# Optimization experiments

Measured on AMD Instinct MI355X. Metric: run time of the kernel, lower is better.

Reference implementation:

```python
import jax, jax.numpy as jnp
import numpy as np

N_AA, N_CG = 262144, 65536
F_AA, F_CG = 16, 32
H = 128
E_CC, E_CA, E_AC = 262144, 524288, 524288
B = 64  # number of graphs in the batch
LN_EPS = 1e-5


def setup_inputs() -> dict:
    key = jax.random.key(0)
    ks = jax.random.split(key, 32)
    inp = {}
    inp['h_aa0'] = jax.random.normal(ks[0], (N_AA, F_AA), jnp.float32)
    inp['h_cg0'] = jax.random.normal(ks[1], (N_CG, F_CG), jnp.float32)
    inp['src_cc'] = jax.random.randint(ks[2], (E_CC,), 0, N_CG, jnp.int32)
    inp['dst_cc'] = jax.random.randint(ks[3], (E_CC,), 0, N_CG, jnp.int32)
    inp['src_ca'] = jax.random.randint(ks[4], (E_CA,), 0, N_CG, jnp.int32)
    inp['dst_ca'] = jax.random.randint(ks[5], (E_CA,), 0, N_AA, jnp.int32)
    inp['src_ac'] = jax.random.randint(ks[6], (E_AC,), 0, N_AA, jnp.int32)
    inp['dst_ac'] = jax.random.randint(ks[7], (E_AC,), 0, N_CG, jnp.int32)
    inp['graph_id'] = jnp.sort(jax.random.randint(ks[8], (N_AA,), 0, B, jnp.int32))
    def W(k, fi, fo):
        return jax.random.normal(k, (fi, fo), jnp.float32) * 0.05
    z = lambda n: jnp.zeros((n,), jnp.float32)
    o = lambda n: jnp.ones((n,), jnp.float32)
    # input MLPs (no skip)
    inp['W_cg0'], inp['b_cg0'], inp['g_cg0'], inp['be_cg0'] = W(ks[9], F_CG, H), z(H), o(H), z(H)
    inp['W_aa0'], inp['b_aa0'], inp['g_aa0'], inp['be_aa0'] = W(ks[10], F_AA, H), z(H), o(H), z(H)
    # GraphConv cg_to_cg
    inp['W_cc'], inp['b_cc'] = W(ks[11], H, H), z(H)
    # nodewise MLP (applied to aa due to source bug), skip connection
    inp['W_m1'], inp['b_m1'], inp['g_m1'], inp['be_m1'] = W(ks[12], H, H), z(H), o(H), z(H)
    # GraphConv cg_to_aa
    inp['W_ca'], inp['b_ca'] = W(ks[13], H, H), z(H)
    # nodewise MLP on aa, skip
    inp['W_m2'], inp['b_m2'], inp['g_m2'], inp['be_m2'] = W(ks[14], H, H), z(H), o(H), z(H)
    # GraphConv aa_to_cg
    inp['W_ac'], inp['b_ac'] = W(ks[15], H, H), z(H)
    # final nodewise MLP on aa (activation None, LN)
    inp['W_f'], inp['b_f'], inp['g_f'], inp['be_f'] = W(ks[16], H, H), z(H), o(H), z(H)
    return inp


def _layer_norm(h, g, be):
    mu = h.mean(-1, keepdims=True)
    var = ((h - mu) ** 2).mean(-1, keepdims=True)
    return (h - mu) * jax.lax.rsqrt(var + LN_EPS) * g + be


def _mlp(x, Wt, b, g, be, act=True, skip=False):
    h = x @ Wt + b
    if act:
        h = jax.nn.elu(h)
    if skip:
        h = h + x
    return _layer_norm(h, g, be)


def _gconv(h_src, src, dst, n_src, n_dst, Wt, b):
    # DGL GraphConv, norm='both': D_dst^{-1/2} A D_src^{-1/2} X W + b, ELU
    ones = jnp.ones(src.shape[0], h_src.dtype)
    d_out = jnp.clip(jax.ops.segment_sum(ones, src, num_segments=n_src), 1.0) ** -0.5
    d_in = jnp.clip(jax.ops.segment_sum(ones, dst, num_segments=n_dst), 1.0) ** -0.5
    msg = (h_src * d_out[:, None])[src]          # [E, H] gather
    agg = jax.ops.segment_sum(msg, dst, num_segments=n_dst)  # [n_dst, H] scatter-add
    return jax.nn.elu((agg * d_in[:, None]) @ Wt + b)


def reference(h_aa0, h_cg0, src_cc, dst_cc, src_ca, dst_ca, src_ac, dst_ac, graph_id,
              W_cg0, b_cg0, g_cg0, be_cg0, W_aa0, b_aa0, g_aa0, be_aa0,
              W_cc, b_cc, W_m1, b_m1, g_m1, be_m1, W_ca, b_ca,
              W_m2, b_m2, g_m2, be_m2, W_ac, b_ac, W_f, b_f, g_f, be_f):
    n_aa, n_cg = h_aa0.shape[0], h_cg0.shape[0]
    # input embedding MLPs
    h_cg = _mlp(h_cg0, W_cg0, b_cg0, g_cg0, be_cg0)
    h_aa = _mlp(h_aa0, W_aa0, b_aa0, g_aa0, be_aa0)
    # cg_to_cg conv (+ identity skip from HeteroGraphConv sum aggregate)
    h_cg = _gconv(h_cg, src_cc, dst_cc, n_cg, n_cg, W_cc, b_cc) + h_cg
    # 'cg' nodewise MLP — applied to aa nodes (source bug reproduced)
    h_aa = _mlp(h_aa, W_m1, b_m1, g_m1, be_m1, skip=True)
    # cg_to_aa conv
    h_aa = _gconv(h_cg, src_ca, dst_ca, n_cg, n_aa, W_ca, b_ca) + h_aa
    # 'aa' nodewise MLP
    h_aa = _mlp(h_aa, W_m2, b_m2, g_m2, be_m2, skip=True)
    # aa_to_cg conv
    h_cg = _gconv(h_aa, src_ac, dst_ac, n_aa, n_cg, W_ac, b_ac) + h_cg
    # final nodewise layer on pooling level 'aa' (no activation, LN)
    h_aa = _mlp(h_aa, W_f, b_f, g_f, be_f, act=False)
    # mean pooling per graph
    sums = jax.ops.segment_sum(h_aa, graph_id, num_segments=B)      # [B, H]
    counts = jax.ops.segment_sum(jnp.ones((n_aa, 1), h_aa.dtype), graph_id, num_segments=B)
    out = sums / jnp.clip(counts, 1.0)
    return out, counts
```

## Files before the change

kernel.cpp:

```cpp
#include <hip/hip_runtime.h>

using ushort = unsigned short;

#define DEVFN static __device__ __forceinline__

constexpr int H = 128;
constexpr int N_AA = 262144, N_CG = 65536;
constexpr int E_CC = 262144, E_CA = 524288;
constexpr int B_GR = 64;

typedef __attribute__((ext_vector_type(8))) short bf16x8;
typedef __attribute__((ext_vector_type(4))) float f32x4;

DEVFN float elu(float x) { return x > 0.f ? x : __expf(x) - 1.f; }

DEVFN float bf2f(ushort s) { return __uint_as_float(((unsigned)s) << 16); }
DEVFN ushort f2bf(float f) {
  unsigned u = __float_as_uint(f);
  return (ushort)((u + 0x7FFFu + ((u >> 16) & 1u)) >> 16);
}
DEVFN ushort4 pack4(const f32x4& a) {
  return make_ushort4(f2bf(a[0]), f2bf(a[1]), f2bf(a[2]), f2bf(a[3]));
}

DEVFN void fma4(float4& c, float a, float4 w) {
  c.x += a * w.x; c.y += a * w.y; c.z += a * w.z; c.w += a * w.w;
}

__global__ void hist4_kernel(const int* __restrict__ src_cc, const int* __restrict__ dst_cc,
                             const int* __restrict__ src_ca, const int* __restrict__ dst_ca,
                             int* __restrict__ c_scc, int* __restrict__ c_dcc,
                             int* __restrict__ c_sca, int* __restrict__ c_dca) {
  int i = blockIdx.x * blockDim.x + threadIdx.x;
  int stride = gridDim.x * blockDim.x;
  const int T = 2 * E_CC + 2 * E_CA;
  for (; i < T; i += stride) {
    const int* a; int* c; int j = i;
    if (j < E_CC) { a = src_cc; c = c_scc; }
    else if (j < 2 * E_CC) { a = dst_cc; c = c_dcc; j -= E_CC; }
    else if (j < 2 * E_CC + E_CA) { a = src_ca; c = c_sca; j -= 2 * E_CC; }
    else { a = dst_ca; c = c_dca; j -= 2 * E_CC + E_CA; }
    atomicAdd(&c[a[j]], 1);
  }
}

__global__ void graph_count_kernel(const int* __restrict__ gid, int n, int* __restrict__ counts) {
  int b = threadIdx.x;
  auto lb = [&](int v) {
    int lo = 0, hi = n;
    while (lo < hi) { int m = (lo + hi) >> 1; if (gid[m] < v) lo = m + 1; else hi = m; }
    return lo;
  };
  int s = lb(b), e = lb(b + 1);
  counts[b] = e - s;
}

__global__ void deg_all_kernel(const int* __restrict__ cnt, float* __restrict__ d) {
  int i = blockIdx.x * blockDim.x + threadIdx.x;
  int c = cnt[i]; if (c < 1) c = 1;
  d[i] = rsqrtf((float)c);
}

__global__ void wprep_kernel(const float* __restrict__ w0, const float* __restrict__ w1,
                             const float* __restrict__ w2, const float* __restrict__ w3,
                             const float* __restrict__ w4,
                             ushort* __restrict__ o0, ushort* __restrict__ o1,
                             ushort* __restrict__ o2, ushort* __restrict__ o3,
                             ushort* __restrict__ o4,
                             const float* __restrict__ wa, ushort* __restrict__ oa) {
  int idx = blockIdx.x * 256 + threadIdx.x;
  if (idx < 81920) {
    int which = idx >> 14, id = idx & 16383;
    const float* W = which == 0 ? w0 : which == 1 ? w1 : which == 2 ? w2 : which == 3 ? w3 : w4;
    ushort* O = which == 0 ? o0 : which == 1 ? o1 : which == 2 ? o2 : which == 3 ? o3 : o4;
    int r = id >> 7, j = id & 127;
    int k = (j - ((r & 15) << 3)) & 127;
    O[id] = f2bf(W[k * 128 + r]);
  } else if (idx < 86016) {
    int id = idx - 81920;
    int n = id >> 5, k = id & 31;
    oa[id] = (k < 16) ? f2bf(wa[k * 128 + n]) : (ushort)0;
  }
}

__global__ void scan1_kernel(const int* __restrict__ in_cc, int* __restrict__ out_cc,
                             const int* __restrict__ in_ca, int* __restrict__ out_ca,
                             int* __restrict__ bsum) {
  __shared__ int l[256];
  int b = blockIdx.x, tid = threadIdx.x;
  const int* in; int* out; int bi;
  if (b < 64) { in = in_cc; out = out_cc; bi = b; } else { in = in_ca; out = out_ca; bi = b - 64; }
  int base = bi * 1024 + tid * 4;
  int4 v = *(const int4*)&in[base];
  int s = v.x + v.y + v.z + v.w;
  l[tid] = s; __syncthreads();
  for (int off = 1; off < 256; off <<= 1) {
    int t = (tid >= off) ? l[tid - off] : 0;
    __syncthreads();
    if (tid >= off) l[tid] += t;
    __syncthreads();
  }
  int excl = l[tid] - s;
  if (tid == 255) bsum[b] = l[255];
  int4 o; o.x = excl; o.y = o.x + v.x; o.z = o.y + v.y; o.w = o.z + v.z;
  *(int4*)&out[base] = o;
}

__global__ void scan2_kernel(int* __restrict__ bsum) {
  __shared__ int l[256];
  int b = blockIdx.x, tid = threadIdx.x;
  int* bs = bsum + (b ? 64 : 0);
  int nb = b ? 256 : 64;
  int v = (tid < nb) ? bs[tid] : 0;
  l[tid] = v; __syncthreads();
  for (int off = 1; off < 256; off <<= 1) {
    int t = (tid >= off) ? l[tid - off] : 0;
    __syncthreads();
    if (tid >= off) l[tid] += t;
    __syncthreads();
  }
  if (tid < nb) bs[tid] = l[tid] - v;
}

__global__ void scan3_kernel(int* __restrict__ offs_cc, int* __restrict__ cur_cc,
                             int* __restrict__ offs_ca, int* __restrict__ cur_ca,
                             const int* __restrict__ bsum) {
  int i = blockIdx.x * blockDim.x + threadIdx.x;
  if (i < N_CG) {
    int o = offs_cc[i] + bsum[i >> 10];
    offs_cc[i] = o; cur_cc[i] = o;
  } else if (i < N_CG + N_AA) {
    int j = i - N_CG;
    int o = offs_ca[j] + bsum[64 + (j >> 10)];
    offs_ca[j] = o; cur_ca[j] = o;
  }
}

__global__ void place2_kernel(const int* __restrict__ src_cc, const int* __restrict__ dst_cc,
                              const int* __restrict__ src_ca, const int* __restrict__ dst_ca,
                              int* __restrict__ cur_cc, int* __restrict__ sorted_cc,
                              int* __restrict__ cur_ca, int* __restrict__ sorted_ca) {
  int i = blockIdx.x * blockDim.x + threadIdx.x;
  int stride = gridDim.x * blockDim.x;
  for (; i < E_CC + E_CA; i += stride) {
    if (i < E_CC) {
      int d = dst_cc[i];
      int slot = atomicAdd(&cur_cc[d], 1);
      sorted_cc[slot] = src_cc[i];
    } else {
      int j = i - E_CC;
      int d = dst_ca[j];
      int slot = atomicAdd(&cur_ca[d], 1);
      sorted_ca[slot] = src_ca[j];
    }
  }
}

__global__ __launch_bounds__(256) void gather_kernel(
    const ushort* __restrict__ h, const int* __restrict__ sorted_src,
    const int* __restrict__ offs, const int* __restrict__ cnt,
    const float* __restrict__ dout, const float* __restrict__ din,
    ushort* __restrict__ out, int ndst) {
  int lane = threadIdx.x & 31;
  int g0 = (blockIdx.x * blockDim.x + threadIdx.x) >> 5;
  int gstride = (gridDim.x * blockDim.x) >> 5;
  for (int d = g0; d < ndst; d += gstride) {
    int o = offs[d], c = cnt[d];
    float ax = 0.f, ay = 0.f, az = 0.f, aw = 0.f;
    for (int e = o; e < o + c; ++e) {
      int s = sorted_src[e];
      float w = dout[s];
      ushort4 u = *(const ushort4*)&h[(size_t)s * H + lane * 4];
      ax += w * bf2f(u.x); ay += w * bf2f(u.y);
      az += w * bf2f(u.z); aw += w * bf2f(u.w);
    }
    float di = din[d];
    ushort4 r = make_ushort4(f2bf(ax * di), f2bf(ay * di), f2bf(az * di), f2bf(aw * di));
    *(ushort4*)&out[(size_t)d * H + lane * 4] = r;
  }
}


DEVFN void stage_w(const ushort* __restrict__ g, ushort* l, int tid) {
  for (int i = tid; i < 2048; i += 512)
    *((uint4*)l + i) = *((const uint4*)g + i);
}

DEVFN void load_bfrag(const ushort* __restrict__ A, size_t mrow, int q, bf16x8 bfr[4]) {
#pragma unroll
  for (int ks = 0; ks < 4; ks++)
    bfr[ks] = *(const bf16x8*)(A + mrow + ks * 32 + q * 8);
}

DEVFN void load_skip_raw(const ushort* __restrict__ skip, size_t mrow, int q, ushort4 sk[8]) {
#pragma unroll
  for (int nf = 0; nf < 8; nf++)
    sk[nf] = *(const ushort4*)&skip[mrow + nf * 16 + q * 4];
}

DEVFN void gemm128_lds(const ushort* __restrict__ Wlds, const bf16x8 bfr[4], f32x4 acc[8], int t, int q) {
#pragma unroll
  for (int ks = 0; ks < 4; ks++) {
    int coff = (ks * 64 + q * 16 + t * 16) & 255;
#pragma unroll
    for (int nf = 0; nf < 8; nf++) {
      bf16x8 wv = *(const bf16x8*)((const char*)Wlds + (nf * 16 + t) * 256 + coff);
      acc[nf] = __builtin_amdgcn_mfma_f32_16x16x32_bf16(wv, bfr[ks], acc[nf], 0, 0, 0);
    }
  }
}

DEVFN void chained_gemm(const ushort* __restrict__ Wlds, char* cbb, int t, int q,
                        const f32x4 ain[8], f32x4 acc[8]) {
  const int tb = t * 8;
  char* row = cbb + t * 128;
#pragma unroll
  for (int half = 0; half < 2; half++) {
    asm volatile("s_waitcnt lgkmcnt(0)" ::: "memory");
#pragma unroll
    for (int nfl = 0; nfl < 4; nfl++) {
      int off = (nfl * 32 + q * 8 + tb) & 127;
      *(ushort4*)(row + off) = pack4(ain[half * 4 + nfl]);
    }
    asm volatile("s_waitcnt lgkmcnt(0)" ::: "memory");
#pragma unroll
    for (int ksl = 0; ksl < 2; ksl++) {
      int ks = half * 2 + ksl;
      uint2 lo = *(const uint2*)(row + ((ksl * 64 + q * 16 + tb) & 127));
      uint2 hi = *(const uint2*)(row + ((ksl * 64 + q * 16 + 8 + tb) & 127));
      union { uint4 u; bf16x8 v; } b;
      b.u = make_uint4(lo.x, lo.y, hi.x, hi.y);
      int coff = (ks * 64 + q * 16 + t * 16) & 255;
#pragma unroll
      for (int nf = 0; nf < 8; nf++) {
        bf16x8 wv = *(const bf16x8*)((const char*)Wlds + (nf * 16 + t) * 256 + coff);
        acc[nf] = __builtin_amdgcn_mfma_f32_16x16x32_bf16(wv, b.v, acc[nf], 0, 0, 0);
      }
    }
  }
}

template<bool ACT>
DEVFN void bias_act(f32x4 a[8], const float* __restrict__ bias, int q) {
#pragma unroll
  for (int nf = 0; nf < 8; nf++) {
    float4 bb = *(const float4*)&bias[nf * 16 + q * 4];
    a[nf][0] += bb.x; a[nf][1] += bb.y; a[nf][2] += bb.z; a[nf][3] += bb.w;
    if constexpr (ACT) {
#pragma unroll
      for (int e = 0; e < 4; e++) a[nf][e] = elu(a[nf][e]);
    }
  }
}

DEVFN void add_reg(f32x4 a[8], const f32x4 b[8]) {
#pragma unroll
  for (int nf = 0; nf < 8; nf++)
#pragma unroll
    for (int e = 0; e < 4; e++) a[nf][e] += b[nf][e];
}

DEVFN void add_skip_r(f32x4 a[8], const ushort4 sk[8]) {
#pragma unroll
  for (int nf = 0; nf < 8; nf++) {
    a[nf][0] += bf2f(sk[nf].x); a[nf][1] += bf2f(sk[nf].y);
    a[nf][2] += bf2f(sk[nf].z); a[nf][3] += bf2f(sk[nf].w);
  }
}

DEVFN void layernorm(f32x4 a[8], const float* __restrict__ gamma, const float* __restrict__ beta, int q) {
  float s = 0.f;
#pragma unroll
  for (int nf = 0; nf < 8; nf++) s += a[nf][0] + a[nf][1] + a[nf][2] + a[nf][3];
  s += __shfl_xor(s, 16); s += __shfl_xor(s, 32);
  float mu = s * 0.0078125f;
  float d = 0.f;
#pragma unroll
  for (int nf = 0; nf < 8; nf++)
#pragma unroll
    for (int e = 0; e < 4; e++) { float x = a[nf][e] - mu; d += x * x; }
  d += __shfl_xor(d, 16); d += __shfl_xor(d, 32);
  float rs = rsqrtf(d * 0.0078125f + 1e-5f);
#pragma unroll
  for (int nf = 0; nf < 8; nf++) {
    float4 gg = *(const float4*)&gamma[nf * 16 + q * 4];
    float4 be = *(const float4*)&beta[nf * 16 + q * 4];
    a[nf][0] = (a[nf][0] - mu) * rs * gg.x + be.x;
    a[nf][1] = (a[nf][1] - mu) * rs * gg.y + be.y;
    a[nf][2] = (a[nf][2] - mu) * rs * gg.z + be.z;
    a[nf][3] = (a[nf][3] - mu) * rs * gg.w + be.w;
  }
}

DEVFN void store_row(ushort* __restrict__ out, size_t mrow, const f32x4 a[8], int q) {
#pragma unroll
  for (int nf = 0; nf < 8; nf++)
    *(ushort4*)&out[mrow + nf * 16 + q * 4] = pack4(a[nf]);
}

__global__ __launch_bounds__(512) void fused_aa_kernel(
    const float* __restrict__ h0, int ngrp,
    const ushort* __restrict__ Wp,
    const float* __restrict__ b0, const float* __restrict__ g0, const float* __restrict__ be0,
    const ushort* __restrict__ Wswm1,
    const float* __restrict__ b1, const float* __restrict__ g1, const float* __restrict__ be1,
    ushort* __restrict__ out) {
  __shared__ ushort Wm1[16384];
  __shared__ ushort chain[8 * 1024];
  int tid = threadIdx.x;
  stage_w(Wswm1, Wm1, tid);
  int lane = tid & 63, wave = tid >> 6;
  int t = lane & 15, q = lane >> 4;
  char* cbb = (char*)chain + wave * 2048;
  bf16x8 wfa[8];
#pragma unroll
  for (int nf = 0; nf < 8; nf++)
    wfa[nf] = *(const bf16x8*)(Wp + (nf * 16 + t) * 32 + q * 8);

  int grp = blockIdx.x;
  float4 c0, c1;
  if (grp < ngrp && q < 2) {
    const float* src = h0 + ((size_t)(grp * 128 + wave * 16 + t) << 4) + (q << 3);
    c0 = *(const float4*)src; c1 = *(const float4*)(src + 4);
  }
  __syncthreads();

  for (; grp < ngrp;) {
    int nxt = grp + gridDim.x;
    float4 n0, n1;
    if (nxt < ngrp && q < 2) {
      const float* src = h0 + ((size_t)(nxt * 128 + wave * 16 + t) << 4) + (q << 3);
      n0 = *(const float4*)src; n1 = *(const float4*)(src + 4);
    }
    size_t mrow = (size_t)(grp * 128 + wave * 16 + t) * H;
    bf16x8 bf0;
    if (q < 2) {
      bf0[0] = (short)f2bf(c0.x); bf0[1] = (short)f2bf(c0.y);
      bf0[2] = (short)f2bf(c0.z); bf0[3] = (short)f2bf(c0.w);
      bf0[4] = (short)f2bf(c1.x); bf0[5] = (short)f2bf(c1.y);
      bf0[6] = (short)f2bf(c1.z); bf0[7] = (short)f2bf(c1.w);
    } else {
#pragma unroll
      for (int e = 0; e < 8; e++) bf0[e] = 0;
    }
    f32x4 a0[8];
#pragma unroll
    for (int nf = 0; nf < 8; nf++) a0[nf] = (f32x4){0.f, 0.f, 0.f, 0.f};
#pragma unroll
    for (int nf = 0; nf < 8; nf++)
      a0[nf] = __builtin_amdgcn_mfma_f32_16x16x32_bf16(wfa[nf], bf0, a0[nf], 0, 0, 0);
    bias_act<true>(a0, b0, q);
    layernorm(a0, g0, be0, q);

    f32x4 a1[8];
#pragma unroll
    for (int nf = 0; nf < 8; nf++) a1[nf] = (f32x4){0.f, 0.f, 0.f, 0.f};
    chained_gemm(Wm1, cbb, t, q, a0, a1);
    bias_act<true>(a1, b1, q);
    add_reg(a1, a0);
    layernorm(a1, g1, be1, q);
    store_row(out, mrow, a1, q);

    grp = nxt; c0 = n0; c1 = n1;
  }
}

__global__ __launch_bounds__(512) void cc_gemm_kernel(
    const ushort* __restrict__ A, int ngrp,
    const ushort* __restrict__ Wsw, const float* __restrict__ bias,
    const ushort* __restrict__ skip, ushort* __restrict__ out) {
  __shared__ ushort Wl[16384];
  int tid = threadIdx.x;
  stage_w(Wsw, Wl, tid);
  int lane = tid & 63, wave = tid >> 6;
  int t = lane & 15, q = lane >> 4;
  __syncthreads();
  for (int grp = blockIdx.x; grp < ngrp; grp += gridDim.x) {
    size_t mrow = (size_t)(grp * 128 + wave * 16 + t) * H;
    bf16x8 bfr[4];
    load_bfrag(A, mrow, q, bfr);
    ushort4 sk[8];
    load_skip_raw(skip, mrow, q, sk);
    f32x4 a[8];
#pragma unroll
    for (int nf = 0; nf < 8; nf++) a[nf] = (f32x4){0.f, 0.f, 0.f, 0.f};
    gemm128_lds(Wl, bfr, a, t, q);
    bias_act<true>(a, bias, q);
    add_skip_r(a, sk);
    store_row(out, mrow, a, q);
  }
}

__global__ __launch_bounds__(512) void fused3_kernel(
    const ushort* __restrict__ A, const ushort* __restrict__ Hbskip, int ngrp,
    const ushort* __restrict__ Wswca, const float* __restrict__ bca,
    const ushort* __restrict__ Wswm2, const float* __restrict__ bm2,
    const float* __restrict__ gm2, const float* __restrict__ bem2,
    const ushort* __restrict__ Wswf, const float* __restrict__ bf,
    const float* __restrict__ gf, const float* __restrict__ bef,
    ushort* __restrict__ out) {
  __shared__ ushort Wca[16384], Wm2[16384], Wf[16384];
  __shared__ ushort chain[8 * 1024];
  int tid = threadIdx.x;
  stage_w(Wswca, Wca, tid);
  stage_w(Wswm2, Wm2, tid);
  stage_w(Wswf, Wf, tid);
  int lane = tid & 63, wave = tid >> 6;
  int t = lane & 15, q = lane >> 4;
  char* cbb = (char*)chain + wave * 2048;

  int grp = blockIdx.x;
  bf16x8 bfr[4];
  ushort4 sk[8];
  if (grp < ngrp) {
    size_t mrow = (size_t)(grp * 128 + wave * 16 + t) * H;
    load_bfrag(A, mrow, q, bfr);
    load_skip_raw(Hbskip, mrow, q, sk);
  }
  __syncthreads();

  for (; grp < ngrp;) {
    int nxt = grp + gridDim.x;
    bf16x8 nbfr[4];
    ushort4 nsk[8];
    if (nxt < ngrp) {
      size_t nrow = (size_t)(nxt * 128 + wave * 16 + t) * H;
      load_bfrag(A, nrow, q, nbfr);
      load_skip_raw(Hbskip, nrow, q, nsk);
    }
    size_t mrow = (size_t)(grp * 128 + wave * 16 + t) * H;

    f32x4 a1[8];
#pragma unroll
    for (int nf = 0; nf < 8; nf++) a1[nf] = (f32x4){0.f, 0.f, 0.f, 0.f};
    gemm128_lds(Wca, bfr, a1, t, q);
    bias_act<true>(a1, bca, q);
    add_skip_r(a1, sk);

    f32x4 a2[8];
#pragma unroll
    for (int nf = 0; nf < 8; nf++) a2[nf] = (f32x4){0.f, 0.f, 0.f, 0.f};
    chained_gemm(Wm2, cbb, t, q, a1, a2);
    bias_act<true>(a2, bm2, q);
    add_reg(a2, a1);
    layernorm(a2, gm2, bem2, q);

    f32x4 a3[8];
#pragma unroll
    for (int nf = 0; nf < 8; nf++) a3[nf] = (f32x4){0.f, 0.f, 0.f, 0.f};
    chained_gemm(Wf, cbb, t, q, a2, a3);
    bias_act<false>(a3, bf, q);
    layernorm(a3, gf, bef, q);
    store_row(out, mrow, a3, q);

    grp = nxt;
#pragma unroll
    for (int ks = 0; ks < 4; ks++) bfr[ks] = nbfr[ks];
#pragma unroll
    for (int nf = 0; nf < 8; nf++) sk[nf] = nsk[nf];
  }
}

template<int K, bool ACT, bool LN>
__global__ __launch_bounds__(512) void gemm_fused(
    const float* __restrict__ Av, int ntiles,
    const float* __restrict__ W, const float* __restrict__ bias,
    const float* __restrict__ gamma, const float* __restrict__ beta,
    ushort* __restrict__ out) {
  constexpr int AS = K + 4;
  constexpr int KM = K - 1;
  constexpr int F4R = K / 4;
  __shared__ float Wl[K * H];
  __shared__ float Al[128 * AS];
  int tid = threadIdx.x;

  for (int q = tid; q < K * H / 4; q += 512)
    *(float4*)&Wl[q * 4] = *(const float4*)&W[q * 4];

  int tc = tid & 31, tr = tid >> 5;
  const int rot = (4 * tr) & KM;
  const int c = 4 * tc;
  const float* aBase = Al + (tr * 8) * AS;

  for (int tile = blockIdx.x; tile < ntiles; tile += gridDim.x) {
    int r0 = tile * 128;
    __syncthreads();
    for (int q = tid; q < 128 * F4R; q += 512) {
      int r = q / F4R, cc = (q % F4R) * 4;
      float4 v = *(const float4*)(Av + (size_t)(r0 + r) * K + cc);
      int rr = (4 * (r >> 3)) & KM;
      *(float4*)&Al[r * AS + ((cc + rr) & KM)] = v;
    }
    __syncthreads();

    float4 acc[8];
#pragma unroll
    for (int i = 0; i < 8; i++) acc[i] = make_float4(0.f, 0.f, 0.f, 0.f);

#pragma unroll 2
    for (int k = 0; k < K; k += 4) {
      int kp = (k + rot) & KM;
      float4 av[8];
#pragma unroll
      for (int r8 = 0; r8 < 8; r8++) av[r8] = *(const float4*)(aBase + r8 * AS + kp);
      float4 w0 = *(const float4*)&Wl[(k + 0) * H + c];
      float4 w1 = *(const float4*)&Wl[(k + 1) * H + c];
      float4 w2 = *(const float4*)&Wl[(k + 2) * H + c];
      float4 w3 = *(const float4*)&Wl[(k + 3) * H + c];
#pragma unroll
      for (int r8 = 0; r8 < 8; r8++) {
        float4 a = av[r8];
        fma4(acc[r8], a.x, w0); fma4(acc[r8], a.y, w1);
        fma4(acc[r8], a.z, w2); fma4(acc[r8], a.w, w3);
      }
    }

    float4 bA = *(const float4*)&bias[c];
    float4 gA, beA;
    if constexpr (LN) {
      gA = *(const float4*)&gamma[c];
      beA = *(const float4*)&beta[c];
    }
#pragma unroll
    for (int r8 = 0; r8 < 8; r8++) {
      int r = tr * 8 + r8;
      size_t grow = (size_t)(r0 + r) * H;
      float4 v;
      v.x = acc[r8].x + bA.x; v.y = acc[r8].y + bA.y;
      v.z = acc[r8].z + bA.z; v.w = acc[r8].w + bA.w;
      if constexpr (ACT) {
        v.x = elu(v.x); v.y = elu(v.y); v.z = elu(v.z); v.w = elu(v.w);
      }
      if constexpr (LN) {
        float s = v.x + v.y + v.z + v.w;
        s += __shfl_xor(s, 1); s += __shfl_xor(s, 2);
        s += __shfl_xor(s, 4); s += __shfl_xor(s, 8); s += __shfl_xor(s, 16);
        float mu = s * 0.0078125f;
        float t, d;
        t = v.x - mu; d = t * t;  t = v.y - mu; d += t * t;
        t = v.z - mu; d += t * t; t = v.w - mu; d += t * t;
        d += __shfl_xor(d, 1); d += __shfl_xor(d, 2);
        d += __shfl_xor(d, 4); d += __shfl_xor(d, 8); d += __shfl_xor(d, 16);
        float rs = rsqrtf(d * 0.0078125f + 1e-5f);
        v.x = (v.x - mu) * rs * gA.x + beA.x; v.y = (v.y - mu) * rs * gA.y + beA.y;
        v.z = (v.z - mu) * rs * gA.z + beA.z; v.w = (v.w - mu) * rs * gA.w + beA.w;
      }
      *(ushort4*)&out[grow + c] = make_ushort4(f2bf(v.x), f2bf(v.y), f2bf(v.z), f2bf(v.w));
    }
  }
}

__global__ __launch_bounds__(128) void pool_sum_kernel(const ushort* __restrict__ h,
                                                       const int* __restrict__ gid,
                                                       float* __restrict__ sums) {
  int f = threadIdx.x;
  int chunk = N_AA / gridDim.x;
  int start = blockIdx.x * chunk, end = start + chunk;
  int g = gid[start];
  float acc = 0.f;
  for (int i = start; i < end; ++i) {
    int gi = gid[i];
    if (gi != g) { atomicAdd(&sums[g * H + f], acc); acc = 0.f; g = gi; }
    acc += bf2f(h[(size_t)i * H + f]);
  }
  atomicAdd(&sums[g * H + f], acc);
}

__global__ void pool_final_kernel(const float* __restrict__ sums, const int* __restrict__ counts,
                                  float* __restrict__ out) {
  int b = blockIdx.x, f = threadIdx.x;
  float c = (float)counts[b];
  out[b * H + f] = sums[b * H + f] / fmaxf(c, 1.f);
  if (f == 0) out[B_GR * H + b] = c;
}

extern "C" void kernel_launch(void* const* d_in, const int* in_sizes, int n_in,
                              void* d_out, int out_size, void* d_ws, size_t ws_size,
                              hipStream_t stream) {
  (void)in_sizes; (void)n_in; (void)out_size; (void)ws_size;
  const float* h_aa0 = (const float*)d_in[0];
  const float* h_cg0 = (const float*)d_in[1];
  const int* src_cc = (const int*)d_in[2];
  const int* dst_cc = (const int*)d_in[3];
  const int* src_ca = (const int*)d_in[4];
  const int* dst_ca = (const int*)d_in[5];
  const int* graph_id = (const int*)d_in[8];
  const float* W_cg0 = (const float*)d_in[9];
  const float* b_cg0 = (const float*)d_in[10];
  const float* g_cg0 = (const float*)d_in[11];
  const float* be_cg0 = (const float*)d_in[12];
  const float* W_aa0 = (const float*)d_in[13];
  const float* b_aa0 = (const float*)d_in[14];
  const float* g_aa0 = (const float*)d_in[15];
  const float* be_aa0 = (const float*)d_in[16];
  const float* W_cc = (const float*)d_in[17];
  const float* b_cc = (const float*)d_in[18];
  const float* W_m1 = (const float*)d_in[19];
  const float* b_m1 = (const float*)d_in[20];
  const float* g_m1 = (const float*)d_in[21];
  const float* be_m1 = (const float*)d_in[22];
  const float* W_ca = (const float*)d_in[23];
  const float* b_ca = (const float*)d_in[24];
  const float* W_m2 = (const float*)d_in[25];
  const float* b_m2 = (const float*)d_in[26];
  const float* g_m2 = (const float*)d_in[27];
  const float* be_m2 = (const float*)d_in[28];
  const float* W_f = (const float*)d_in[31];
  const float* b_f = (const float*)d_in[32];
  const float* g_f = (const float*)d_in[33];
  const float* be_f = (const float*)d_in[34];

  char* ws = (char*)d_ws;
  size_t off = 0;
  auto alloc = [&](size_t bytes) -> void* {
    void* p = ws + off;
    off = (off + bytes + 255) & ~(size_t)255;
    return p;
  };
  ushort* cgA = (ushort*)alloc((size_t)N_CG * H * 2);
  ushort* G   = (ushort*)alloc((size_t)N_CG * H * 2);
  ushort* Hb  = (ushort*)alloc((size_t)N_AA * H * 2);
  ushort* AGG = (ushort*)alloc((size_t)N_AA * H * 2);
  int* cnt_s_cc = (int*)alloc((size_t)N_CG * 4);
  int* cnt_d_cc = (int*)alloc((size_t)N_CG * 4);
  int* cnt_s_ca = (int*)alloc((size_t)N_CG * 4);
  int* cnt_d_ca = (int*)alloc((size_t)N_AA * 4);
  float* dout_cc = (float*)alloc((size_t)N_CG * 4);
  float* din_cc  = (float*)alloc((size_t)N_CG * 4);
  float* dout_ca = (float*)alloc((size_t)N_CG * 4);
  float* din_ca  = (float*)alloc((size_t)N_AA * 4);
  int* offs_cc = (int*)alloc((size_t)N_CG * 4);
  int* cur_cc  = (int*)alloc((size_t)N_CG * 4);
  int* offs_ca = (int*)alloc((size_t)N_AA * 4);
  int* cur_ca  = (int*)alloc((size_t)N_AA * 4);
  int* sorted_cc = (int*)alloc((size_t)E_CC * 4);
  int* sorted_ca = (int*)alloc((size_t)E_CA * 4);
  int* bsum = (int*)alloc(320 * 4);
  float* sums = (float*)alloc((size_t)B_GR * H * 4);
  int* counts = (int*)alloc(256);
  ushort* Wsw_cc = (ushort*)alloc(H * H * 2);
  ushort* Wsw_m1 = (ushort*)alloc(H * H * 2);
  ushort* Wsw_ca = (ushort*)alloc(H * H * 2);
  ushort* Wsw_m2 = (ushort*)alloc(H * H * 2);
  ushort* Wsw_f  = (ushort*)alloc(H * H * 2);
  ushort* Wp_aa  = (ushort*)alloc(H * 32 * 2);

  hipMemsetAsync(cnt_s_cc, 0, (size_t)(3 * N_CG + N_AA) * 4, stream);
  hipMemsetAsync(sums, 0, (size_t)B_GR * H * 4, stream);

  wprep_kernel<<<336, 256, 0, stream>>>(W_cc, W_m1, W_ca, W_m2, W_f,
                                        Wsw_cc, Wsw_m1, Wsw_ca, Wsw_m2, Wsw_f,
                                        W_aa0, Wp_aa);
  hist4_kernel<<<2048, 256, 0, stream>>>(src_cc, dst_cc, src_ca, dst_ca,
                                         cnt_s_cc, cnt_d_cc, cnt_s_ca, cnt_d_ca);
  graph_count_kernel<<<1, 64, 0, stream>>>(graph_id, N_AA, counts);
  deg_all_kernel<<<(3 * N_CG + N_AA) / 256, 256, 0, stream>>>(cnt_s_cc, dout_cc);

  scan1_kernel<<<320, 256, 0, stream>>>(cnt_d_cc, offs_cc, cnt_d_ca, offs_ca, bsum);
  scan2_kernel<<<2, 256, 0, stream>>>(bsum);
  scan3_kernel<<<(N_CG + N_AA) / 256, 256, 0, stream>>>(offs_cc, cur_cc, offs_ca, cur_ca, bsum);
  place2_kernel<<<2048, 256, 0, stream>>>(src_cc, dst_cc, src_ca, dst_ca,
                                          cur_cc, sorted_cc, cur_ca, sorted_ca);

  gemm_fused<32, true, true><<<N_CG / 128, 512, 0, stream>>>(
      h_cg0, N_CG / 128, W_cg0, b_cg0, g_cg0, be_cg0, cgA);

  fused_aa_kernel<<<512, 512, 0, stream>>>(
      h_aa0, N_AA / 128, Wp_aa, b_aa0, g_aa0, be_aa0,
      Wsw_m1, b_m1, g_m1, be_m1, Hb);

  gather_kernel<<<N_CG / 8, 256, 0, stream>>>(cgA, sorted_cc, offs_cc, cnt_d_cc, dout_cc, din_cc, G, N_CG);
  cc_gemm_kernel<<<N_CG / 128, 512, 0, stream>>>(G, N_CG / 128, Wsw_cc, b_cc, cgA, G);

  gather_kernel<<<N_AA / 8, 256, 0, stream>>>(G, sorted_ca, offs_ca, cnt_d_ca, dout_ca, din_ca, AGG, N_AA);
  fused3_kernel<<<256, 512, 0, stream>>>(
      AGG, Hb, N_AA / 128,
      Wsw_ca, b_ca, Wsw_m2, b_m2, g_m2, be_m2,
      Wsw_f, b_f, g_f, be_f, AGG);

  pool_sum_kernel<<<1024, 128, 0, stream>>>(AGG, graph_id, sums);
  pool_final_kernel<<<B_GR, 128, 0, stream>>>(sums, counts, (float*)d_out);
}
```

Before: 476.7 us.

## Process two 16-row tiles per wave to reuse LDS weight fragments

Each wave now handles 32 rows instead of 16 in the aa-embedding, cc GEMM and fused3 kernels, so every weight fragment read from LDS feeds two MFMAs, halving LDS weight traffic per row. Chain buffers double to hold both tiles. The fused_aa kernel drops its register prefetch of the next group's input, and fused3 now loads the skip values inside the loop instead of prefetching them. Register pressure roughly doubles for accumulators, which risks lower occupancy or spills. Grid sizes are adjusted accordingly (fused_aa grid raised to 1024 blocks).

```diff
diff --git a/kernel.cpp b/kernel.cpp
--- a/kernel.cpp
+++ b/kernel.cpp
@@ -198,43 +198,56 @@
     sk[nf] = *(const ushort4*)&skip[mrow + nf * 16 + q * 4];
 }
 
-DEVFN void gemm128_lds(const ushort* __restrict__ Wlds, const bf16x8 bfr[4], f32x4 acc[8], int t, int q) {
+DEVFN void gemm128_lds2(const ushort* __restrict__ Wlds,
+                        const bf16x8 b0[4], const bf16x8 b1[4],
+                        f32x4 A0[8], f32x4 A1[8], int t, int q) {
 #pragma unroll
   for (int ks = 0; ks < 4; ks++) {
     int coff = (ks * 64 + q * 16 + t * 16) & 255;
 #pragma unroll
     for (int nf = 0; nf < 8; nf++) {
       bf16x8 wv = *(const bf16x8*)((const char*)Wlds + (nf * 16 + t) * 256 + coff);
-      acc[nf] = __builtin_amdgcn_mfma_f32_16x16x32_bf16(wv, bfr[ks], acc[nf], 0, 0, 0);
-    }
-  }
-}
-
-DEVFN void chained_gemm(const ushort* __restrict__ Wlds, char* cbb, int t, int q,
-                        const f32x4 ain[8], f32x4 acc[8]) {
+      A0[nf] = __builtin_amdgcn_mfma_f32_16x16x32_bf16(wv, b0[ks], A0[nf], 0, 0, 0);
+      A1[nf] = __builtin_amdgcn_mfma_f32_16x16x32_bf16(wv, b1[ks], A1[nf], 0, 0, 0);
+    }
+  }
+}
+
+DEVFN void chained_gemm2(const ushort* __restrict__ Wlds, char* cb0, char* cb1,
+                         int t, int q,
+                         const f32x4 i0[8], const f32x4 i1[8],
+                         f32x4 A0[8], f32x4 A1[8]) {
   const int tb = t * 8;
-  char* row = cbb + t * 128;
+  char* row0 = cb0 + t * 128;
+  char* row1 = cb1 + t * 128;
 #pragma unroll
   for (int half = 0; half < 2; half++) {
     asm volatile("s_waitcnt lgkmcnt(0)" ::: "memory");
 #pragma unroll
     for (int nfl = 0; nfl < 4; nfl++) {
       int off = (nfl * 32 + q * 8 + tb) & 127;
-      *(ushort4*)(row + off) = pack4(ain[half * 4 + nfl]);
+      *(ushort4*)(row0 + off) = pack4(i0[half * 4 + nfl]);
+      *(ushort4*)(row1 + off) = pack4(i1[half * 4 + nfl]);
     }
     asm volatile("s_waitcnt lgkmcnt(0)" ::: "memory");
 #pragma unroll
     for (int ksl = 0; ksl < 2; ksl++) {
       int ks = half * 2 + ksl;
-      uint2 lo = *(const uint2*)(row + ((ksl * 64 + q * 16 + tb) & 127));
-      uint2 hi = *(const uint2*)(row + ((ksl * 64 + q * 16 + 8 + tb) & 127));
-      union { uint4 u; bf16x8 v; } b;
-      b.u = make_uint4(lo.x, lo.y, hi.x, hi.y);
+      int olo = (ksl * 64 + q * 16 + tb) & 127;
+      int ohi = (ksl * 64 + q * 16 + 8 + tb) & 127;
+      uint2 lo0 = *(const uint2*)(row0 + olo);
+      uint2 hi0 = *(const uint2*)(row0 + ohi);
+      uint2 lo1 = *(const uint2*)(row1 + olo);
+      uint2 hi1 = *(const uint2*)(row1 + ohi);
+      union { uint4 u; bf16x8 v; } b0, b1;
+      b0.u = make_uint4(lo0.x, lo0.y, hi0.x, hi0.y);
+      b1.u = make_uint4(lo1.x, lo1.y, hi1.x, hi1.y);
       int coff = (ks * 64 + q * 16 + t * 16) & 255;
 #pragma unroll
       for (int nf = 0; nf < 8; nf++) {
         bf16x8 wv = *(const bf16x8*)((const char*)Wlds + (nf * 16 + t) * 256 + coff);
-        acc[nf] = __builtin_amdgcn_mfma_f32_16x16x32_bf16(wv, b.v, acc[nf], 0, 0, 0);
+        A0[nf] = __builtin_amdgcn_mfma_f32_16x16x32_bf16(wv, b0.v, A0[nf], 0, 0, 0);
+        A1[nf] = __builtin_amdgcn_mfma_f32_16x16x32_bf16(wv, b1.v, A1[nf], 0, 0, 0);
       }
     }
   }
@@ -306,62 +319,70 @@
     const float* __restrict__ b1, const float* __restrict__ g1, const float* __restrict__ be1,
     ushort* __restrict__ out) {
   __shared__ ushort Wm1[16384];
-  __shared__ ushort chain[8 * 1024];
+  __shared__ ushort chain[8 * 2048];
   int tid = threadIdx.x;
   stage_w(Wswm1, Wm1, tid);
   int lane = tid & 63, wave = tid >> 6;
   int t = lane & 15, q = lane >> 4;
-  char* cbb = (char*)chain + wave * 2048;
+  char* cb0 = (char*)chain + wave * 4096;
+  char* cb1 = cb0 + 2048;
   bf16x8 wfa[8];
 #pragma unroll
   for (int nf = 0; nf < 8; nf++)
     wfa[nf] = *(const bf16x8*)(Wp + (nf * 16 + t) * 32 + q * 8);
-
-  int grp = blockIdx.x;
-  float4 c0, c1;
-  if (grp < ngrp && q < 2) {
-    const float* src = h0 + ((size_t)(grp * 128 + wave * 16 + t) << 4) + (q << 3);
-    c0 = *(const float4*)src; c1 = *(const float4*)(src + 4);
-  }
   __syncthreads();
 
-  for (; grp < ngrp;) {
-    int nxt = grp + gridDim.x;
-    float4 n0, n1;
-    if (nxt < ngrp && q < 2) {
-      const float* src = h0 + ((size_t)(nxt * 128 + wave * 16 + t) << 4) + (q << 3);
-      n0 = *(const float4*)src; n1 = *(const float4*)(src + 4);
-    }
-    size_t mrow = (size_t)(grp * 128 + wave * 16 + t) * H;
-    bf16x8 bf0;
-    if (q < 2) {
-      bf0[0] = (short)f2bf(c0.x); bf0[1] = (short)f2bf(c0.y);
-      bf0[2] = (short)f2bf(c0.z); bf0[3] = (short)f2bf(c0.w);
-      bf0[4] = (short)f2bf(c1.x); bf0[5] = (short)f2bf(c1.y);
-      bf0[6] = (short)f2bf(c1.z); bf0[7] = (short)f2bf(c1.w);
-    } else {
-#pragma unroll
-      for (int e = 0; e < 8; e++) bf0[e] = 0;
-    }
-    f32x4 a0[8];
-#pragma unroll
-    for (int nf = 0; nf < 8; nf++) a0[nf] = (f32x4){0.f, 0.f, 0.f, 0.f};
-#pragma unroll
-    for (int nf = 0; nf < 8; nf++)
-      a0[nf] = __builtin_amdgcn_mfma_f32_16x16x32_bf16(wfa[nf], bf0, a0[nf], 0, 0, 0);
-    bias_act<true>(a0, b0, q);
-    layernorm(a0, g0, be0, q);
-
-    f32x4 a1[8];
-#pragma unroll
-    for (int nf = 0; nf < 8; nf++) a1[nf] = (f32x4){0.f, 0.f, 0.f, 0.f};
-    chained_gemm(Wm1, cbb, t, q, a0, a1);
-    bias_act<true>(a1, b1, q);
-    add_reg(a1, a0);
-    layernorm(a1, g1, be1, q);
-    store_row(out, mrow, a1, q);
-
-    grp = nxt; c0 = n0; c1 = n1;
+  for (int grp = blockIdx.x; grp < ngrp; grp += gridDim.x) {
+    int base = grp * 256 + wave * 32;
+    size_t mrow0 = (size_t)(base + t) * H;
+    size_t mrow1 = (size_t)(base + 16 + t) * H;
+
+    bf16x8 bf0[2];
+#pragma unroll
+    for (int g = 0; g < 2; g++) {
+      if (q < 2) {
+        const float* src = h0 + ((size_t)(base + g * 16 + t) << 4) + (q << 3);
+        float4 u0 = *(const float4*)src;
+        float4 u1 = *(const float4*)(src + 4);
+        bf0[g][0] = (short)f2bf(u0.x); bf0[g][1] = (short)f2bf(u0.y);
+        bf0[g][2] = (short)f2bf(u0.z); bf0[g][3] = (short)f2bf(u0.w);
+        bf0[g][4] = (short)f2bf(u1.x); bf0[g][5] = (short)f2bf(u1.y);
+        bf0[g][6] = (short)f2bf(u1.z); bf0[g][7] = (short)f2bf(u1.w);
+      } else {
+#pragma unroll
+        for (int e = 0; e < 8; e++) bf0[g][e] = 0;
+      }
+    }
+    f32x4 a0[2][8];
+#pragma unroll
+    for (int g = 0; g < 2; g++)
+#pragma unroll
+      for (int nf = 0; nf < 8; nf++) a0[g][nf] = (f32x4){0.f, 0.f, 0.f, 0.f};
+#pragma unroll
+    for (int nf = 0; nf < 8; nf++) {
+      a0[0][nf] = __builtin_amdgcn_mfma_f32_16x16x32_bf16(wfa[nf], bf0[0], a0[0][nf], 0, 0, 0);
+      a0[1][nf] = __builtin_amdgcn_mfma_f32_16x16x32_bf16(wfa[nf], bf0[1], a0[1][nf], 0, 0, 0);
+    }
+#pragma unroll
+    for (int g = 0; g < 2; g++) {
+      bias_act<true>(a0[g], b0, q);
+      layernorm(a0[g], g0, be0, q);
+    }
+
+    f32x4 a1[2][8];
+#pragma unroll
+    for (int g = 0; g < 2; g++)
+#pragma unroll
+      for (int nf = 0; nf < 8; nf++) a1[g][nf] = (f32x4){0.f, 0.f, 0.f, 0.f};
+    chained_gemm2(Wm1, cb0, cb1, t, q, a0[0], a0[1], a1[0], a1[1]);
+#pragma unroll
+    for (int g = 0; g < 2; g++) {
+      bias_act<true>(a1[g], b1, q);
+      add_reg(a1[g], a0[g]);
+      layernorm(a1[g], g1, be1, q);
+    }
+    store_row(out, mrow0, a1[0], q);
+    store_row(out, mrow1, a1[1], q);
   }
 }
 
@@ -376,18 +397,28 @@
   int t = lane & 15, q = lane >> 4;
   __syncthreads();
   for (int grp = blockIdx.x; grp < ngrp; grp += gridDim.x) {
-    size_t mrow = (size_t)(grp * 128 + wave * 16 + t) * H;
-    bf16x8 bfr[4];
-    load_bfrag(A, mrow, q, bfr);
-    ushort4 sk[8];
-    load_skip_raw(skip, mrow, q, sk);
-    f32x4 a[8];
-#pragma unroll
-    for (int nf = 0; nf < 8; nf++) a[nf] = (f32x4){0.f, 0.f, 0.f, 0.f};
-    gemm128_lds(Wl, bfr, a, t, q);
-    bias_act<true>(a, bias, q);
-    add_skip_r(a, sk);
-    store_row(out, mrow, a, q);
+    int base = grp * 256 + wave * 32;
+    size_t mrow0 = (size_t)(base + t) * H;
+    size_t mrow1 = (size_t)(base + 16 + t) * H;
+    bf16x8 bfr[2][4];
+    load_bfrag(A, mrow0, q, bfr[0]);
+    load_bfrag(A, mrow1, q, bfr[1]);
+    ushort4 sk[2][8];
+    load_skip_raw(skip, mrow0, q, sk[0]);
+    load_skip_raw(skip, mrow1, q, sk[1]);
+    f32x4 a[2][8];
+#pragma unroll
+    for (int g = 0; g < 2; g++)
+#pragma unroll
+      for (int nf = 0; nf < 8; nf++) a[g][nf] = (f32x4){0.f, 0.f, 0.f, 0.f};
+    gemm128_lds2(Wl, bfr[0], bfr[1], a[0], a[1], t, q);
+#pragma unroll
+    for (int g = 0; g < 2; g++) {
+      bias_act<true>(a[g], bias, q);
+      add_skip_r(a[g], sk[g]);
+    }
+    store_row(out, mrow0, a[0], q);
+    store_row(out, mrow1, a[1], q);
   }
 }
 
@@ -400,64 +431,84 @@
     const float* __restrict__ gf, const float* __restrict__ bef,
     ushort* __restrict__ out) {
   __shared__ ushort Wca[16384], Wm2[16384], Wf[16384];
-  __shared__ ushort chain[8 * 1024];
+  __shared__ ushort chain[8 * 2048];
   int tid = threadIdx.x;
   stage_w(Wswca, Wca, tid);
   stage_w(Wswm2, Wm2, tid);
   stage_w(Wswf, Wf, tid);
   int lane = tid & 63, wave = tid >> 6;
   int t = lane & 15, q = lane >> 4;
-  char* cbb = (char*)chain + wave * 2048;
+  char* cb0 = (char*)chain + wave * 4096;
+  char* cb1 = cb0 + 2048;
 
   int grp = blockIdx.x;
-  bf16x8 bfr[4];
-  ushort4 sk[8];
+  bf16x8 bfr[2][4];
   if (grp < ngrp) {
-    size_t mrow = (size_t)(grp * 128 + wave * 16 + t) * H;
-    load_bfrag(A, mrow, q, bfr);
-    load_skip_raw(Hbskip, mrow, q, sk);
+    int base = grp * 256 + wave * 32;
+    load_bfrag(A, (size_t)(base + t) * H, q, bfr[0]);
+    load_bfrag(A, (size_t)(base + 16 + t) * H, q, bfr[1]);
   }
   __syncthreads();
 
   for (; grp < ngrp;) {
     int nxt = grp + gridDim.x;
-    bf16x8 nbfr[4];
-    ushort4 nsk[8];
+    bf16x8 nbfr[2][4];
     if (nxt < ngrp) {
-      size_t nrow = (size_t)(nxt * 128 + wave * 16 + t) * H;
-      load_bfrag(A, nrow, q, nbfr);
-      load_skip_raw(Hbskip, nrow, q, nsk);
-    }
-    size_t mrow = (size_t)(grp * 128 + wave * 16 + t) * H;
-
-    f32x4 a1[8];
-#pragma unroll
-    for (int nf = 0; nf < 8; nf++) a1[nf] = (f32x4){0.f, 0.f, 0.f, 0.f};
-    gemm128_lds(Wca, bfr, a1, t, q);
-    bias_act<true>(a1, bca, q);
-    add_skip_r(a1, sk);
-
-    f32x4 a2[8];
-#pragma unroll
-    for (int nf = 0; nf < 8; nf++) a2[nf] = (f32x4){0.f, 0.f, 0.f, 0.f};
-    chained_gemm(Wm2, cbb, t, q, a1, a2);
-    bias_act<true>(a2, bm2, q);
-    add_reg(a2, a1);
-    layernorm(a2, gm2, bem2, q);
-
-    f32x4 a3[8];
-#pragma unroll
-    for (int nf = 0; nf < 8; nf++) a3[nf] = (f32x4){0.f, 0.f, 0.f, 0.f};
-    chained_gemm(Wf, cbb, t, q, a2, a3);
-    bias_act<false>(a3, bf, q);
-    layernorm(a3, gf, bef, q);
-    store_row(out, mrow, a3, q);
+      int nb = nxt * 256 + wave * 32;
+      load_bfrag(A, (size_t)(nb + t) * H, q, nbfr[0]);
+      load_bfrag(A, (size_t)(nb + 16 + t) * H, q, nbfr[1]);
+    }
+    int base = grp * 256 + wave * 32;
+    size_t mrow0 = (size_t)(base + t) * H;
+    size_t mrow1 = (size_t)(base + 16 + t) * H;
+    ushort4 sk[2][8];
+    load_skip_raw(Hbskip, mrow0, q, sk[0]);
+    load_skip_raw(Hbskip, mrow1, q, sk[1]);
+
+    f32x4 a1[2][8];
+#pragma unroll
+    for (int g = 0; g < 2; g++)
+#pragma unroll
+      for (int nf = 0; nf < 8; nf++) a1[g][nf] = (f32x4){0.f, 0.f, 0.f, 0.f};
+    gemm128_lds2(Wca, bfr[0], bfr[1], a1[0], a1[1], t, q);
+#pragma unroll
+    for (int g = 0; g < 2; g++) {
+      bias_act<true>(a1[g], bca, q);
+      add_skip_r(a1[g], sk[g]);
+    }
+
+    f32x4 a2[2][8];
+#pragma unroll
+    for (int g = 0; g < 2; g++)
+#pragma unroll
+      for (int nf = 0; nf < 8; nf++) a2[g][nf] = (f32x4){0.f, 0.f, 0.f, 0.f};
+    chained_gemm2(Wm2, cb0, cb1, t, q, a1[0], a1[1], a2[0], a2[1]);
+#pragma unroll
+    for (int g = 0; g < 2; g++) {
+      bias_act<true>(a2[g], bm2, q);
+      add_reg(a2[g], a1[g]);
+      layernorm(a2[g], gm2, bem2, q);
+    }
+
+    f32x4 a3[2][8];
+#pragma unroll
+    for (int g = 0; g < 2; g++)
+#pragma unroll
+      for (int nf = 0; nf < 8; nf++) a3[g][nf] = (f32x4){0.f, 0.f, 0.f, 0.f};
+    chained_gemm2(Wf, cb0, cb1, t, q, a2[0], a2[1], a3[0], a3[1]);
+#pragma unroll
+    for (int g = 0; g < 2; g++) {
+      bias_act<false>(a3[g], bf, q);
+      layernorm(a3[g], gf, bef, q);
+    }
+    store_row(out, mrow0, a3[0], q);
+    store_row(out, mrow1, a3[1], q);
 
     grp = nxt;
 #pragma unroll
-    for (int ks = 0; ks < 4; ks++) bfr[ks] = nbfr[ks];
-#pragma unroll
-    for (int nf = 0; nf < 8; nf++) sk[nf] = nsk[nf];
+    for (int g = 0; g < 2; g++)
+#pragma unroll
+      for (int ks = 0; ks < 4; ks++) bfr[g][ks] = nbfr[g][ks];
   }
 }
 
@@ -665,16 +716,16 @@
   gemm_fused<32, true, true><<<N_CG / 128, 512, 0, stream>>>(
       h_cg0, N_CG / 128, W_cg0, b_cg0, g_cg0, be_cg0, cgA);
 
-  fused_aa_kernel<<<512, 512, 0, stream>>>(
-      h_aa0, N_AA / 128, Wp_aa, b_aa0, g_aa0, be_aa0,
+  fused_aa_kernel<<<1024, 512, 0, stream>>>(
+      h_aa0, N_AA / 256, Wp_aa, b_aa0, g_aa0, be_aa0,
       Wsw_m1, b_m1, g_m1, be_m1, Hb);
 
   gather_kernel<<<N_CG / 8, 256, 0, stream>>>(cgA, sorted_cc, offs_cc, cnt_d_cc, dout_cc, din_cc, G, N_CG);
-  cc_gemm_kernel<<<N_CG / 128, 512, 0, stream>>>(G, N_CG / 128, Wsw_cc, b_cc, cgA, G);
+  cc_gemm_kernel<<<N_CG / 256, 512, 0, stream>>>(G, N_CG / 256, Wsw_cc, b_cc, cgA, G);
 
   gather_kernel<<<N_AA / 8, 256, 0, stream>>>(G, sorted_ca, offs_ca, cnt_d_ca, dout_ca, din_ca, AGG, N_AA);
   fused3_kernel<<<256, 512, 0, stream>>>(
-      AGG, Hb, N_AA / 128,
+      AGG, Hb, N_AA / 256,
       Wsw_ca, b_ca, Wsw_m2, b_m2, g_m2, be_m2,
       Wsw_f, b_f, g_f, be_f, AGG);
 
```

Measured after the change: 559.7 us. 17.4% more time.

## Fuse neighbor gather into conv GEMM kernels and split the aa MLP chain

Applied to the files above, without the earlier changes.

The separate gather kernels are removed. Each destination row's neighbor sum is now built directly in MFMA B-fragment registers inside the cc and ca GEMM kernels, so the aggregated tensor is no longer written to and re-read from memory. The old three-GEMM fused kernel is split into a ca conv kernel and a separate m2+final MLP kernel, which lowers LDS use per block but adds a round trip of the intermediate activations through global memory. It also adds s_setprio around the MFMA loops and raises the grid sizes for the aa MLP and pool kernels. The fused gather has one thread per row doing serial neighbor loops with 32 accumulators, which can cost parallelism, add register pressure and cause load imbalance.

```diff
diff --git a/kernel.cpp b/kernel.cpp
--- a/kernel.cpp
+++ b/kernel.cpp
@@ -156,30 +156,6 @@
   }
 }
 
-__global__ __launch_bounds__(256) void gather_kernel(
-    const ushort* __restrict__ h, const int* __restrict__ sorted_src,
-    const int* __restrict__ offs, const int* __restrict__ cnt,
-    const float* __restrict__ dout, const float* __restrict__ din,
-    ushort* __restrict__ out, int ndst) {
-  int lane = threadIdx.x & 31;
-  int g0 = (blockIdx.x * blockDim.x + threadIdx.x) >> 5;
-  int gstride = (gridDim.x * blockDim.x) >> 5;
-  for (int d = g0; d < ndst; d += gstride) {
-    int o = offs[d], c = cnt[d];
-    float ax = 0.f, ay = 0.f, az = 0.f, aw = 0.f;
-    for (int e = o; e < o + c; ++e) {
-      int s = sorted_src[e];
-      float w = dout[s];
-      ushort4 u = *(const ushort4*)&h[(size_t)s * H + lane * 4];
-      ax += w * bf2f(u.x); ay += w * bf2f(u.y);
-      az += w * bf2f(u.z); aw += w * bf2f(u.w);
-    }
-    float di = din[d];
-    ushort4 r = make_ushort4(f2bf(ax * di), f2bf(ay * di), f2bf(az * di), f2bf(aw * di));
-    *(ushort4*)&out[(size_t)d * H + lane * 4] = r;
-  }
-}
-
 
 DEVFN void stage_w(const ushort* __restrict__ g, ushort* l, int tid) {
   for (int i = tid; i < 2048; i += 512)
@@ -198,7 +174,33 @@
     sk[nf] = *(const ushort4*)&skip[mrow + nf * 16 + q * 4];
 }
 
+DEVFN void gather_bfrag(const ushort* __restrict__ h, const int* __restrict__ sorted,
+                        int o, int c, const float* __restrict__ dout, float di,
+                        int q, bf16x8 bfr[4]) {
+  float acc[4][8];
+#pragma unroll
+  for (int ks = 0; ks < 4; ks++)
+#pragma unroll
+    for (int j = 0; j < 8; j++) acc[ks][j] = 0.f;
+  for (int e = o; e < o + c; ++e) {
+    int s = sorted[e];
+    float w = dout[s];
+    const ushort* row = h + (size_t)s * H + q * 8;
+#pragma unroll
+    for (int ks = 0; ks < 4; ks++) {
+      bf16x8 v = *(const bf16x8*)(row + ks * 32);
+#pragma unroll
+      for (int j = 0; j < 8; j++) acc[ks][j] += w * bf2f((ushort)v[j]);
+    }
+  }
+#pragma unroll
+  for (int ks = 0; ks < 4; ks++)
+#pragma unroll
+    for (int j = 0; j < 8; j++) bfr[ks][j] = (short)f2bf(acc[ks][j] * di);
+}
+
 DEVFN void gemm128_lds(const ushort* __restrict__ Wlds, const bf16x8 bfr[4], f32x4 acc[8], int t, int q) {
+  __builtin_amdgcn_s_setprio(1);
 #pragma unroll
   for (int ks = 0; ks < 4; ks++) {
     int coff = (ks * 64 + q * 16 + t * 16) & 255;
@@ -208,6 +210,7 @@
       acc[nf] = __builtin_amdgcn_mfma_f32_16x16x32_bf16(wv, bfr[ks], acc[nf], 0, 0, 0);
     }
   }
+  __builtin_amdgcn_s_setprio(0);
 }
 
 DEVFN void chained_gemm(const ushort* __restrict__ Wlds, char* cbb, int t, int q,
@@ -231,11 +234,13 @@
       union { uint4 u; bf16x8 v; } b;
       b.u = make_uint4(lo.x, lo.y, hi.x, hi.y);
       int coff = (ks * 64 + q * 16 + t * 16) & 255;
+      __builtin_amdgcn_s_setprio(1);
 #pragma unroll
       for (int nf = 0; nf < 8; nf++) {
         bf16x8 wv = *(const bf16x8*)((const char*)Wlds + (nf * 16 + t) * 256 + coff);
         acc[nf] = __builtin_amdgcn_mfma_f32_16x16x32_bf16(wv, b.v, acc[nf], 0, 0, 0);
       }
+      __builtin_amdgcn_s_setprio(0);
     }
   }
 }
@@ -346,9 +351,11 @@
     f32x4 a0[8];
 #pragma unroll
     for (int nf = 0; nf < 8; nf++) a0[nf] = (f32x4){0.f, 0.f, 0.f, 0.f};
+    __builtin_amdgcn_s_setprio(1);
 #pragma unroll
     for (int nf = 0; nf < 8; nf++)
       a0[nf] = __builtin_amdgcn_mfma_f32_16x16x32_bf16(wfa[nf], bf0, a0[nf], 0, 0, 0);
+    __builtin_amdgcn_s_setprio(0);
     bias_act<true>(a0, b0, q);
     layernorm(a0, g0, be0, q);
 
@@ -365,10 +372,13 @@
   }
 }
 
-__global__ __launch_bounds__(512) void cc_gemm_kernel(
-    const ushort* __restrict__ A, int ngrp,
+__global__ __launch_bounds__(512) void cc_fused_kernel(
+    const ushort* __restrict__ cgA, int ngrp,
+    const int* __restrict__ offs, const int* __restrict__ cnt,
+    const int* __restrict__ sorted, const float* __restrict__ dout,
+    const float* __restrict__ din,
     const ushort* __restrict__ Wsw, const float* __restrict__ bias,
-    const ushort* __restrict__ skip, ushort* __restrict__ out) {
+    ushort* __restrict__ outG) {
   __shared__ ushort Wl[16384];
   int tid = threadIdx.x;
   stage_w(Wsw, Wl, tid);
@@ -376,73 +386,82 @@
   int t = lane & 15, q = lane >> 4;
   __syncthreads();
   for (int grp = blockIdx.x; grp < ngrp; grp += gridDim.x) {
-    size_t mrow = (size_t)(grp * 128 + wave * 16 + t) * H;
+    int nd = grp * 128 + wave * 16 + t;
+    size_t mrow = (size_t)nd * H;
     bf16x8 bfr[4];
-    load_bfrag(A, mrow, q, bfr);
+    gather_bfrag(cgA, sorted, offs[nd], cnt[nd], dout, din[nd], q, bfr);
     ushort4 sk[8];
-    load_skip_raw(skip, mrow, q, sk);
+    load_skip_raw(cgA, mrow, q, sk);
     f32x4 a[8];
 #pragma unroll
     for (int nf = 0; nf < 8; nf++) a[nf] = (f32x4){0.f, 0.f, 0.f, 0.f};
     gemm128_lds(Wl, bfr, a, t, q);
     bias_act<true>(a, bias, q);
     add_skip_r(a, sk);
-    store_row(out, mrow, a, q);
-  }
-}
-
-__global__ __launch_bounds__(512) void fused3_kernel(
-    const ushort* __restrict__ A, const ushort* __restrict__ Hbskip, int ngrp,
-    const ushort* __restrict__ Wswca, const float* __restrict__ bca,
+    store_row(outG, mrow, a, q);
+  }
+}
+
+__global__ __launch_bounds__(512) void ca_fused_kernel(
+    const ushort* __restrict__ G, const ushort* __restrict__ Hbskip, int ngrp,
+    const int* __restrict__ offs, const int* __restrict__ cnt,
+    const int* __restrict__ sorted, const float* __restrict__ dout,
+    const float* __restrict__ din,
+    const ushort* __restrict__ Wsw, const float* __restrict__ bias,
+    ushort* __restrict__ outX) {
+  __shared__ ushort Wl[16384];
+  int tid = threadIdx.x;
+  stage_w(Wsw, Wl, tid);
+  int lane = tid & 63, wave = tid >> 6;
+  int t = lane & 15, q = lane >> 4;
+  __syncthreads();
+  for (int grp = blockIdx.x; grp < ngrp; grp += gridDim.x) {
+    int nd = grp * 128 + wave * 16 + t;
+    size_t mrow = (size_t)nd * H;
+    bf16x8 bfr[4];
+    gather_bfrag(G, sorted, offs[nd], cnt[nd], dout, din[nd], q, bfr);
+    ushort4 sk[8];
+    load_skip_raw(Hbskip, mrow, q, sk);
+    f32x4 a[8];
+#pragma unroll
+    for (int nf = 0; nf < 8; nf++) a[nf] = (f32x4){0.f, 0.f, 0.f, 0.f};
+    gemm128_lds(Wl, bfr, a, t, q);
+    bias_act<true>(a, bias, q);
+    add_skip_r(a, sk);
+    store_row(outX, mrow, a, q);
+  }
+}
+
+__global__ __launch_bounds__(512) void m2f_kernel(
+    const ushort* __restrict__ X, int ngrp,
     const ushort* __restrict__ Wswm2, const float* __restrict__ bm2,
     const float* __restrict__ gm2, const float* __restrict__ bem2,
     const ushort* __restrict__ Wswf, const float* __restrict__ bf,
     const float* __restrict__ gf, const float* __restrict__ bef,
     ushort* __restrict__ out) {
-  __shared__ ushort Wca[16384], Wm2[16384], Wf[16384];
+  __shared__ ushort Wm2[16384], Wf[16384];
   __shared__ ushort chain[8 * 1024];
   int tid = threadIdx.x;
-  stage_w(Wswca, Wca, tid);
   stage_w(Wswm2, Wm2, tid);
   stage_w(Wswf, Wf, tid);
   int lane = tid & 63, wave = tid >> 6;
   int t = lane & 15, q = lane >> 4;
   char* cbb = (char*)chain + wave * 2048;
-
-  int grp = blockIdx.x;
-  bf16x8 bfr[4];
-  ushort4 sk[8];
-  if (grp < ngrp) {
+  __syncthreads();
+
+  for (int grp = blockIdx.x; grp < ngrp; grp += gridDim.x) {
     size_t mrow = (size_t)(grp * 128 + wave * 16 + t) * H;
-    load_bfrag(A, mrow, q, bfr);
-    load_skip_raw(Hbskip, mrow, q, sk);
-  }
-  __syncthreads();
-
-  for (; grp < ngrp;) {
-    int nxt = grp + gridDim.x;
-    bf16x8 nbfr[4];
-    ushort4 nsk[8];
-    if (nxt < ngrp) {
-      size_t nrow = (size_t)(nxt * 128 + wave * 16 + t) * H;
-      load_bfrag(A, nrow, q, nbfr);
-      load_skip_raw(Hbskip, nrow, q, nsk);
-    }
-    size_t mrow = (size_t)(grp * 128 + wave * 16 + t) * H;
-
-    f32x4 a1[8];
-#pragma unroll
-    for (int nf = 0; nf < 8; nf++) a1[nf] = (f32x4){0.f, 0.f, 0.f, 0.f};
-    gemm128_lds(Wca, bfr, a1, t, q);
-    bias_act<true>(a1, bca, q);
-    add_skip_r(a1, sk);
+    bf16x8 bfr[4];
+    load_bfrag(X, mrow, q, bfr);
+    ushort4 sk[8];
+    load_skip_raw(X, mrow, q, sk);
 
     f32x4 a2[8];
 #pragma unroll
     for (int nf = 0; nf < 8; nf++) a2[nf] = (f32x4){0.f, 0.f, 0.f, 0.f};
-    chained_gemm(Wm2, cbb, t, q, a1, a2);
+    gemm128_lds(Wm2, bfr, a2, t, q);
     bias_act<true>(a2, bm2, q);
-    add_reg(a2, a1);
+    add_skip_r(a2, sk);
     layernorm(a2, gm2, bem2, q);
 
     f32x4 a3[8];
@@ -452,12 +471,6 @@
     bias_act<false>(a3, bf, q);
     layernorm(a3, gf, bef, q);
     store_row(out, mrow, a3, q);
-
-    grp = nxt;
-#pragma unroll
-    for (int ks = 0; ks < 4; ks++) bfr[ks] = nbfr[ks];
-#pragma unroll
-    for (int nf = 0; nf < 8; nf++) sk[nf] = nsk[nf];
   }
 }
 
@@ -665,19 +678,22 @@
   gemm_fused<32, true, true><<<N_CG / 128, 512, 0, stream>>>(
       h_cg0, N_CG / 128, W_cg0, b_cg0, g_cg0, be_cg0, cgA);
 
-  fused_aa_kernel<<<512, 512, 0, stream>>>(
+  fused_aa_kernel<<<768, 512, 0, stream>>>(
       h_aa0, N_AA / 128, Wp_aa, b_aa0, g_aa0, be_aa0,
       Wsw_m1, b_m1, g_m1, be_m1, Hb);
 
-  gather_kernel<<<N_CG / 8, 256, 0, stream>>>(cgA, sorted_cc, offs_cc, cnt_d_cc, dout_cc, din_cc, G, N_CG);
-  cc_gemm_kernel<<<N_CG / 128, 512, 0, stream>>>(G, N_CG / 128, Wsw_cc, b_cc, cgA, G);
-
-  gather_kernel<<<N_AA / 8, 256, 0, stream>>>(G, sorted_ca, offs_ca, cnt_d_ca, dout_ca, din_ca, AGG, N_AA);
-  fused3_kernel<<<256, 512, 0, stream>>>(
-      AGG, Hb, N_AA / 128,
-      Wsw_ca, b_ca, Wsw_m2, b_m2, g_m2, be_m2,
+  cc_fused_kernel<<<N_CG / 128, 512, 0, stream>>>(
+      cgA, N_CG / 128, offs_cc, cnt_d_cc, sorted_cc, dout_cc, din_cc,
+      Wsw_cc, b_cc, G);
+
+  ca_fused_kernel<<<N_AA / 128, 512, 0, stream>>>(
+      G, Hb, N_AA / 128, offs_ca, cnt_d_ca, sorted_ca, dout_ca, din_ca,
+      Wsw_ca, b_ca, AGG);
+
+  m2f_kernel<<<N_AA / 128, 512, 0, stream>>>(
+      AGG, N_AA / 128, Wsw_m2, b_m2, g_m2, be_m2,
       Wsw_f, b_f, g_f, be_f, AGG);
 
-  pool_sum_kernel<<<1024, 128, 0, stream>>>(AGG, graph_id, sums);
+  pool_sum_kernel<<<2048, 128, 0, stream>>>(AGG, graph_id, sums);
   pool_final_kernel<<<B_GR, 128, 0, stream>>>(sums, counts, (float*)d_out);
 }
```

Result: slower. 490.6 us (+2.9%).
